# Kernel tuning notes

Measured on AMD Instinct MI355X. Metric: run time of the kernel, lower is better.

## Reference

```python
import jax, jax.numpy as jnp
import numpy as np

N, E = 50000, 800000
IN_F, OUT_F, EMB, KER = 64, 64, 3, 4


def setup_inputs() -> dict:
    key = jax.random.key(0)
    ks = jax.random.split(key, 6)
    x = jax.random.normal(ks[0], (N, IN_F), dtype=jnp.float32)
    edge_idx = jax.random.randint(ks[1], (2, E), 0, N, dtype=jnp.int64)
    spec_domain = jax.random.normal(ks[2], (N, EMB), dtype=jnp.float32)
    weight = 0.1 * jax.random.normal(ks[3], (IN_F, OUT_F, KER), dtype=jnp.float32)
    bias_p = 0.1 * jax.random.normal(ks[4], (OUT_F,), dtype=jnp.float32)
    mu = 0.005 * jax.random.normal(ks[5], (EMB, KER), dtype=jnp.float32)
    sig = jnp.ones((1, KER), dtype=jnp.float32)  # repo default 60140 underflows exp with random embeddings
    return {"x": x, "edge_idx": edge_idx, "spec_domain": spec_domain,
            "weight": weight, "bias_p": bias_p, "mu": mu, "sig": sig}


def reference(x, edge_idx, spec_domain, weight, bias_p, mu, sig):
    n = x.shape[0]
    row, col = edge_idx[0], edge_idx[1]
    # support for all kernels at once: [N, out, K]
    support = jnp.einsum('ni,iok->nok', x, weight)
    # per-edge Gaussian kernel values: [E, K]
    diff = spec_domain[row] - spec_domain[col]               # [E, emb]
    dm = diff[:, :, None] - mu[None, :, :]                   # [E, emb, K]
    qq = -0.5 * jnp.sum(dm * dm, axis=1)                     # [E, K]
    value = jnp.exp(sig[0][None, :] * qq)                    # [E, K]
    # sparse mm: out[row] += value * support[col], per kernel
    msgs = value[:, None, :] * support[col]                  # [E, out, K]
    out = jax.ops.segment_sum(msgs, row, num_segments=n)     # [N, out, K]
    return out.sum(axis=2) + bias_p
```

## Files before the change

kernel.cpp:

```cpp
#include <hip/hip_runtime.h>
#include <hip/hip_fp16.h>

#define FIN 64
#define CAP 48
#define BINSH 8
#define NBINMAX 256
#define PCAP 5120
#define TILE_B 2048

__global__ __launch_bounds__(256) void p1_kernel(const float* __restrict__ x,
                                                 const float* __restrict__ weight,
                                                 __half* __restrict__ sup,
                                                 const int* __restrict__ eidx,
                                                 int* __restrict__ gcur,
                                                 int* __restrict__ part,
                                                 int n, int e_total, int sblocks) {
    const int t = threadIdx.x;
    __shared__ float xs[32][64];
    __shared__ int hist[NBINMAX], lbase[NBINMAX], gbase[NBINMAX];
    __shared__ int wsum[4];

    const int rowbase = blockIdx.x * 32;
    if (rowbase < n) {
        {
            const float4* __restrict__ x4 = (const float4*)(x + (size_t)rowbase * 64);
            float4* __restrict__ s4 = (float4*)&xs[0][0];
            int limit = (n - rowbase) * 16;
            if (limit > 512) limit = 512;
            #pragma unroll
            for (int j = 0; j < 2; ++j) {
                int idx = t + j * 256;
                if (idx < limit) s4[idx] = x4[idx];
            }
        }
        __syncthreads();

        const int w = t >> 6;
        const int o = t & 63;

        float4 acc[8];
        #pragma unroll
        for (int r = 0; r < 8; ++r) acc[r] = make_float4(0.f, 0.f, 0.f, 0.f);

        #pragma unroll 4
        for (int ic = 0; ic < 16; ++ic) {
            float4 w0 = *(const float4*)&weight[(ic * 4 + 0) * 256 + o * 4];
            float4 w1 = *(const float4*)&weight[(ic * 4 + 1) * 256 + o * 4];
            float4 w2 = *(const float4*)&weight[(ic * 4 + 2) * 256 + o * 4];
            float4 w3 = *(const float4*)&weight[(ic * 4 + 3) * 256 + o * 4];
            #pragma unroll
            for (int r = 0; r < 8; ++r) {
                float4 xv = *(const float4*)&xs[w * 8 + r][ic * 4];
                acc[r].x += xv.x * w0.x + xv.y * w1.x + xv.z * w2.x + xv.w * w3.x;
                acc[r].y += xv.x * w0.y + xv.y * w1.y + xv.z * w2.y + xv.w * w3.y;
                acc[r].z += xv.x * w0.z + xv.y * w1.z + xv.z * w2.z + xv.w * w3.z;
                acc[r].w += xv.x * w0.w + xv.y * w1.w + xv.z * w2.w + xv.w * w3.w;
            }
        }

        #pragma unroll
        for (int r = 0; r < 8; ++r) {
            int gr = rowbase + w * 8 + r;
            if (gr < n) {
                union { __half2 h[2]; uint2 u; } p;
                p.h[0] = __floats2half2_rn(acc[r].x, acc[r].y);
                p.h[1] = __floats2half2_rn(acc[r].z, acc[r].w);
                *(uint2*)&sup[(size_t)gr * 256 + o * 4] = p.u;
            }
        }
    }

    if (blockIdx.x < sblocks) {
        int nz = 0;
        #pragma unroll
        for (int j = 1; j < 16; j += 2) nz |= eidx[j];
        const int is64 = (nz == 0);

        hist[t] = 0;
        __syncthreads();

        const int base = blockIdx.x * TILE_B;
        int nv = e_total - base;
        if (nv > TILE_B) nv = TILE_B;
        if (nv < 0) nv = 0;

        int er[8], ec_[8], lp[8], vb[8];
        #pragma unroll
        for (int i = 0; i < 4; ++i) {
            const int pl = t + 256 * i;
            const int pg = (base >> 1) + pl;
            int r0 = 0, c0 = 0, r1 = 0, c1 = 0, v0 = 0, v1 = 0;
            if (2 * pl < nv) {
                if (is64) {
                    int4 rr = ((const int4*)eidx)[pg];
                    int4 cc = ((const int4*)(eidx + 2 * (size_t)e_total))[pg];
                    r0 = rr.x; c0 = cc.x; v0 = 1;
                    if (2 * pl + 1 < nv) { r1 = rr.z; c1 = cc.z; v1 = 1; }
                } else {
                    int2 rr = ((const int2*)eidx)[pg];
                    int2 cc = ((const int2*)(eidx + (size_t)e_total))[pg];
                    r0 = rr.x; c0 = cc.x; v0 = 1;
                    if (2 * pl + 1 < nv) { r1 = rr.y; c1 = cc.y; v1 = 1; }
                }
            }
            er[2 * i] = r0; ec_[2 * i] = c0; vb[2 * i] = v0;
            er[2 * i + 1] = r1; ec_[2 * i + 1] = c1; vb[2 * i + 1] = v1;
        }
        #pragma unroll
        for (int i = 0; i < 8; ++i) {
            lp[i] = vb[i] ? atomicAdd(&hist[er[i] >> BINSH], 1) : 0;
        }
        __syncthreads();

        {
            const int lane = t & 63;
            const int w = t >> 6;
            int h = hist[t];
            int s = h;
            #pragma unroll
            for (int off = 1; off < 64; off <<= 1) {
                int u = __shfl_up(s, off, 64);
                if (lane >= off) s += u;
            }
            if (lane == 63) wsum[w] = s;
            __syncthreads();
            if (t == 0) {
                int a = 0;
                #pragma unroll
                for (int q = 0; q < 4; ++q) { int u = wsum[q]; wsum[q] = a; a += u; }
            }
            __syncthreads();
            lbase[t] = s - h + wsum[w];
            gbase[t] = (h > 0) ? atomicAdd(&gcur[t], h) : 0;
        }
        __syncthreads();

        #pragma unroll
        for (int i = 0; i < 8; ++i) {
            if (vb[i]) {
                int b = er[i] >> BINSH;
                int dst = gbase[b] + lp[i];
                if (dst < PCAP) part[b * PCAP + dst] = (ec_[i] << 8) | (er[i] & 255);
            }
        }
    }
}

__global__ __launch_bounds__(1024) void p2_kernel(const int* __restrict__ gcur,
                                                  const int* __restrict__ part,
                                                  const float* __restrict__ spec,
                                                  const float* __restrict__ mu,
                                                  const float* __restrict__ sig,
                                                  int* __restrict__ cnt,
                                                  int* __restrict__ scol,
                                                  uint2* __restrict__ sval, int n) {
    __shared__ int cl[256];
    const int t = threadIdx.x;
    const int b = blockIdx.x;
    const int row0 = b << BINSH;
    if (t < 256) cl[t] = 0;
    __syncthreads();

    float m0[4], m1[4], m2[4], sg[4];
    #pragma unroll
    for (int k = 0; k < 4; ++k) {
        m0[k] = mu[k]; m1[k] = mu[4 + k]; m2[k] = mu[8 + k]; sg[k] = sig[k];
    }

    int nloc = gcur[b];
    if (nloc > PCAP) nloc = PCAP;
    const int* __restrict__ mypart = part + b * PCAP;

    for (int i = t; i < nloc; i += 1024) {
        int e = mypart[i];
        int rl = e & 255;
        int col = ((unsigned)e) >> 8;
        int row = row0 + rl;

        float d0 = spec[row * 3 + 0] - spec[col * 3 + 0];
        float d1 = spec[row * 3 + 1] - spec[col * 3 + 1];
        float d2 = spec[row * 3 + 2] - spec[col * 3 + 2];
        float v[4];
        #pragma unroll
        for (int k = 0; k < 4; ++k) {
            float a = d0 - m0[k], bb = d1 - m1[k], c = d2 - m2[k];
            v[k] = __expf(sg[k] * (-0.5f * (a * a + bb * bb + c * c)));
        }
        union { __half2 h; unsigned u; } p01, p23;
        p01.h = __floats2half2_rn(v[0], v[1]);
        p23.h = __floats2half2_rn(v[2], v[3]);

        int pos = atomicAdd(&cl[rl], 1);
        if (pos < CAP) {
            scol[(size_t)row * CAP + pos] = col;
            sval[(size_t)row * CAP + pos] = make_uint2(p01.u, p23.u);
        }
    }
    __syncthreads();

    int row = row0 + t;
    if (t < 256 && row < n) cnt[row] = (cl[t] > CAP) ? CAP : cl[t];
}

__device__ __forceinline__ float dot_supv(uint2 p, uint2 pv) {
    float2 f0 = __half22float2(__builtin_bit_cast(__half2, p.x));
    float2 f1 = __half22float2(__builtin_bit_cast(__half2, p.y));
    float2 a0 = __half22float2(__builtin_bit_cast(__half2, pv.x));
    float2 a1 = __half22float2(__builtin_bit_cast(__half2, pv.y));
    return f0.x * a0.x + f0.y * a0.y + f1.x * a1.x + f1.y * a1.y;
}

__global__ __launch_bounds__(256, 6) void row_kernel(const int* __restrict__ cnt,
                                                     const int* __restrict__ scol,
                                                     const uint2* __restrict__ sval,
                                                     const __half* __restrict__ sup,
                                                     const float* __restrict__ bias,
                                                     float* __restrict__ out, int n) {
    const int lane = threadIdx.x & 63;
    const int wl = threadIdx.x >> 6;
    const int wv = __builtin_amdgcn_readfirstlane(blockIdx.x * 4 + wl);
    const int NW = gridDim.x * 4;
    const float bias_l = bias[lane];
    const unsigned un = (unsigned)n;

    for (int r = wv; r < n; r += NW) {
        int ec = cnt[r];
        if (ec > CAP) ec = CAP;
        const size_t base = (size_t)r * CAP;
        float acc = bias_l;

        for (int j = 0; j < ec; j += 16) {
            int c[16]; uint2 w[16];
            #pragma unroll
            for (int i = 0; i < 16; ++i) {
                int idx = j + i;
                int cc = scol[base + idx];
                uint2 ww = sval[base + idx];
                bool valid = idx < ec;
                c[i] = ((unsigned)cc < un) ? cc : 0;
                w[i] = valid ? ww : make_uint2(0u, 0u);
            }
            uint2 p[16];
            #pragma unroll
            for (int i = 0; i < 16; ++i)
                p[i] = *(const uint2*)(sup + ((size_t)c[i] * 256 + lane * 4));
            #pragma unroll
            for (int i = 0; i < 16; ++i)
                acc += dot_supv(p[i], w[i]);
        }
        out[(size_t)r * 64 + lane] = acc;
    }
}

extern "C" void kernel_launch(void* const* d_in, const int* in_sizes, int n_in,
                              void* d_out, int out_size, void* d_ws, size_t ws_size,
                              hipStream_t stream) {
    const float* x      = (const float*)d_in[0];
    const int*   eidx   = (const int*)d_in[1];
    const float* spec   = (const float*)d_in[2];
    const float* weight = (const float*)d_in[3];
    const float* bias   = (const float*)d_in[4];
    const float* mu     = (const float*)d_in[5];
    const float* sig    = (const float*)d_in[6];
    float* out = (float*)d_out;

    const int N = in_sizes[0] / FIN;
    const int E = in_sizes[1] / 2;
    const int NB32 = (N + 31) / 32;
    const int SBLK = (E + TILE_B - 1) / TILE_B;
    const int GRID1 = (NB32 > SBLK) ? NB32 : SBLK;
    const int NBIN = (N + (1 << BINSH) - 1) >> BINSH;

    char* w = (char*)d_ws;
    size_t off = 0;
    int* gcur = (int*)(w + off);            off += NBINMAX * 4;
    __half* sup = (__half*)(w + off);       off += (size_t)N * 256 * sizeof(__half);
    off = (off + 255) & ~(size_t)255;
    int* cnt = (int*)(w + off);             off += (size_t)N * 4;
    off = (off + 255) & ~(size_t)255;
    int* scol = (int*)(w + off);            off += (size_t)N * CAP * 4;
    off = (off + 255) & ~(size_t)255;
    uint2* sval = (uint2*)(w + off);        off += (size_t)N * CAP * 8;
    off = (off + 255) & ~(size_t)255;
    int* part = (int*)(w + off);            off += (size_t)NBIN * PCAP * 4;

    hipMemsetAsync(gcur, 0, NBINMAX * 4, stream);
    p1_kernel<<<GRID1, 256, 0, stream>>>(x, weight, sup, eidx, gcur, part, N, E, SBLK);
    p2_kernel<<<NBIN, 1024, 0, stream>>>(gcur, part, spec, mu, sig, cnt, scol, sval, N);
    row_kernel<<<1536, 256, 0, stream>>>(cnt, scol, sval, sup, bias, out, N);
}
```

Baseline: 122.6 us.

## Fuse edge-weight computation and row aggregation into one shared-memory consume kernel

Replaces the separate p2 pass, which scattered per-row column and weight lists into padded global arrays, and the row-gather kernel with one kernel. Each block handles a 64-row sub-bin of a 256-row partition. It counts edges per row, prefix-sums offsets, computes the Gaussian weights into a compact CSR in LDS, then aggregates fp16 support rows per wave. This removes the global round trip for scol/sval/cnt and one launch. The cost is that each block scans its whole parent partition twice, so partition reads are repeated 4x. It also adds a per-sub-bin LDS cap of 1536 edges that could truncate dense regions.

```diff
diff --git a/kernel.cpp b/kernel.cpp
--- a/kernel.cpp
+++ b/kernel.cpp
@@ -2,11 +2,11 @@
 #include <hip/hip_fp16.h>
 
 #define FIN 64
-#define CAP 48
 #define BINSH 8
 #define NBINMAX 256
 #define PCAP 5120
 #define TILE_B 2048
+#define SBCAP 1536
 
 __global__ __launch_bounds__(256) void p1_kernel(const float* __restrict__ x,
                                                  const float* __restrict__ weight,
@@ -146,62 +146,6 @@
     }
 }
 
-__global__ __launch_bounds__(1024) void p2_kernel(const int* __restrict__ gcur,
-                                                  const int* __restrict__ part,
-                                                  const float* __restrict__ spec,
-                                                  const float* __restrict__ mu,
-                                                  const float* __restrict__ sig,
-                                                  int* __restrict__ cnt,
-                                                  int* __restrict__ scol,
-                                                  uint2* __restrict__ sval, int n) {
-    __shared__ int cl[256];
-    const int t = threadIdx.x;
-    const int b = blockIdx.x;
-    const int row0 = b << BINSH;
-    if (t < 256) cl[t] = 0;
-    __syncthreads();
-
-    float m0[4], m1[4], m2[4], sg[4];
-    #pragma unroll
-    for (int k = 0; k < 4; ++k) {
-        m0[k] = mu[k]; m1[k] = mu[4 + k]; m2[k] = mu[8 + k]; sg[k] = sig[k];
-    }
-
-    int nloc = gcur[b];
-    if (nloc > PCAP) nloc = PCAP;
-    const int* __restrict__ mypart = part + b * PCAP;
-
-    for (int i = t; i < nloc; i += 1024) {
-        int e = mypart[i];
-        int rl = e & 255;
-        int col = ((unsigned)e) >> 8;
-        int row = row0 + rl;
-
-        float d0 = spec[row * 3 + 0] - spec[col * 3 + 0];
-        float d1 = spec[row * 3 + 1] - spec[col * 3 + 1];
-        float d2 = spec[row * 3 + 2] - spec[col * 3 + 2];
-        float v[4];
-        #pragma unroll
-        for (int k = 0; k < 4; ++k) {
-            float a = d0 - m0[k], bb = d1 - m1[k], c = d2 - m2[k];
-            v[k] = __expf(sg[k] * (-0.5f * (a * a + bb * bb + c * c)));
-        }
-        union { __half2 h; unsigned u; } p01, p23;
-        p01.h = __floats2half2_rn(v[0], v[1]);
-        p23.h = __floats2half2_rn(v[2], v[3]);
-
-        int pos = atomicAdd(&cl[rl], 1);
-        if (pos < CAP) {
-            scol[(size_t)row * CAP + pos] = col;
-            sval[(size_t)row * CAP + pos] = make_uint2(p01.u, p23.u);
-        }
-    }
-    __syncthreads();
-
-    int row = row0 + t;
-    if (t < 256 && row < n) cnt[row] = (cl[t] > CAP) ? CAP : cl[t];
-}
-
 __device__ __forceinline__ float dot_supv(uint2 p, uint2 pv) {
     float2 f0 = __half22float2(__builtin_bit_cast(__half2, p.x));
     float2 f1 = __half22float2(__builtin_bit_cast(__half2, p.y));
@@ -210,33 +154,104 @@
     return f0.x * a0.x + f0.y * a0.y + f1.x * a1.x + f1.y * a1.y;
 }
 
-__global__ __launch_bounds__(256, 6) void row_kernel(const int* __restrict__ cnt,
-                                                     const int* __restrict__ scol,
-                                                     const uint2* __restrict__ sval,
-                                                     const __half* __restrict__ sup,
-                                                     const float* __restrict__ bias,
-                                                     float* __restrict__ out, int n) {
-    const int lane = threadIdx.x & 63;
-    const int wl = threadIdx.x >> 6;
-    const int wv = __builtin_amdgcn_readfirstlane(blockIdx.x * 4 + wl);
-    const int NW = gridDim.x * 4;
+__global__ __launch_bounds__(512) void consume_kernel(const int* __restrict__ gcur,
+                                                      const int* __restrict__ part,
+                                                      const float* __restrict__ spec,
+                                                      const float* __restrict__ mu,
+                                                      const float* __restrict__ sig,
+                                                      const __half* __restrict__ sup,
+                                                      const float* __restrict__ bias,
+                                                      float* __restrict__ out, int n) {
+    __shared__ int   lcol[SBCAP];
+    __shared__ uint2 lval[SBCAP];
+    __shared__ int cl[64], off[64], cl2[64];
+    const int t = threadIdx.x;
+    const int lane = t & 63;
+    const int wl = t >> 6;
+    const int sb = blockIdx.x;
+    const int pb = sb >> 2;
+    const int q  = sb & 3;
+    const int row0 = sb * 64;
+
+    if (t < 64) { cl[t] = 0; cl2[t] = 0; }
+    __syncthreads();
+
+    int nloc = gcur[pb];
+    if (nloc > PCAP) nloc = PCAP;
+    const int* __restrict__ mypart = part + pb * PCAP;
+
+    for (int i = t; i < nloc; i += 512) {
+        int e = mypart[i];
+        int rl = e & 255;
+        if ((rl >> 6) == q) atomicAdd(&cl[rl & 63], 1);
+    }
+    __syncthreads();
+
+    if (wl == 0) {
+        int h = cl[lane];
+        int s = h;
+        #pragma unroll
+        for (int o = 1; o < 64; o <<= 1) {
+            int u = __shfl_up(s, o, 64);
+            if (lane >= o) s += u;
+        }
+        off[lane] = s - h;
+    }
+    __syncthreads();
+
+    float m0[4], m1[4], m2[4], sg[4];
+    #pragma unroll
+    for (int k = 0; k < 4; ++k) {
+        m0[k] = mu[k]; m1[k] = mu[4 + k]; m2[k] = mu[8 + k]; sg[k] = sig[k];
+    }
+
+    for (int i = t; i < nloc; i += 512) {
+        int e = mypart[i];
+        int rl = e & 255;
+        if ((rl >> 6) == q) {
+            int col = ((unsigned)e) >> 8;
+            int rloc = rl & 63;
+            int row = row0 + rloc;
+            float d0 = spec[row * 3 + 0] - spec[col * 3 + 0];
+            float d1 = spec[row * 3 + 1] - spec[col * 3 + 1];
+            float d2 = spec[row * 3 + 2] - spec[col * 3 + 2];
+            float v[4];
+            #pragma unroll
+            for (int k = 0; k < 4; ++k) {
+                float a = d0 - m0[k], bb = d1 - m1[k], c = d2 - m2[k];
+                v[k] = __expf(sg[k] * (-0.5f * (a * a + bb * bb + c * c)));
+            }
+            union { __half2 h; unsigned u; } p01, p23;
+            p01.h = __floats2half2_rn(v[0], v[1]);
+            p23.h = __floats2half2_rn(v[2], v[3]);
+            int pos = off[rloc] + atomicAdd(&cl2[rloc], 1);
+            if (pos < SBCAP) {
+                lcol[pos] = col;
+                lval[pos] = make_uint2(p01.u, p23.u);
+            }
+        }
+    }
+    __syncthreads();
+
     const float bias_l = bias[lane];
     const unsigned un = (unsigned)n;
-
-    for (int r = wv; r < n; r += NW) {
-        int ec = cnt[r];
-        if (ec > CAP) ec = CAP;
-        const size_t base = (size_t)r * CAP;
+    for (int rr = wl; rr < 64; rr += 8) {
+        int row = row0 + rr;
+        if (row >= n) continue;
+        const int s0 = off[rr];
+        int ec = cl[rr];
+        if (s0 + ec > SBCAP) ec = (SBCAP > s0) ? (SBCAP - s0) : 0;
         float acc = bias_l;
 
         for (int j = 0; j < ec; j += 16) {
             int c[16]; uint2 w[16];
             #pragma unroll
             for (int i = 0; i < 16; ++i) {
-                int idx = j + i;
-                int cc = scol[base + idx];
-                uint2 ww = sval[base + idx];
-                bool valid = idx < ec;
+                int idx = s0 + j + i;
+                if (idx > SBCAP - 1) idx = SBCAP - 1;
+                int cc = lcol[idx];
+                uint2 ww = lval[idx];
+                bool valid = (j + i) < ec;
                 c[i] = ((unsigned)cc < un) ? cc : 0;
                 w[i] = valid ? ww : make_uint2(0u, 0u);
             }
@@ -248,7 +263,7 @@
             for (int i = 0; i < 16; ++i)
                 acc += dot_supv(p[i], w[i]);
         }
-        out[(size_t)r * 64 + lane] = acc;
+        out[(size_t)row * 64 + lane] = acc;
     }
 }
 
@@ -268,24 +283,17 @@
     const int E = in_sizes[1] / 2;
     const int NB32 = (N + 31) / 32;
     const int SBLK = (E + TILE_B - 1) / TILE_B;
-    const int GRID1 = (NB32 > SBLK) ? NB32 : SBLK;
     const int NBIN = (N + (1 << BINSH) - 1) >> BINSH;
+    const int NSB  = NBIN * 4;
 
     char* w = (char*)d_ws;
     size_t off = 0;
     int* gcur = (int*)(w + off);            off += NBINMAX * 4;
     __half* sup = (__half*)(w + off);       off += (size_t)N * 256 * sizeof(__half);
     off = (off + 255) & ~(size_t)255;
-    int* cnt = (int*)(w + off);             off += (size_t)N * 4;
-    off = (off + 255) & ~(size_t)255;
-    int* scol = (int*)(w + off);            off += (size_t)N * CAP * 4;
-    off = (off + 255) & ~(size_t)255;
-    uint2* sval = (uint2*)(w + off);        off += (size_t)N * CAP * 8;
-    off = (off + 255) & ~(size_t)255;
     int* part = (int*)(w + off);            off += (size_t)NBIN * PCAP * 4;
 
     hipMemsetAsync(gcur, 0, NBINMAX * 4, stream);
-    p1_kernel<<<GRID1, 256, 0, stream>>>(x, weight, sup, eidx, gcur, part, N, E, SBLK);
-    p2_kernel<<<NBIN, 1024, 0, stream>>>(gcur, part, spec, mu, sig, cnt, scol, sval, N);
-    row_kernel<<<1536, 256, 0, stream>>>(cnt, scol, sval, sup, bias, out, N);
-}
+    p1_kernel<<<NB32, 256, 0, stream>>>(x, weight, sup, eidx, gcur, part, N, E, SBLK);
+    consume_kernel<<<NSB, 512, 0, stream>>>(gcur, part, spec, mu, sig, sup, bias, out, N);
+}
```

Result: slower. 136.2 us (+11.1%).
